# Performance work log

Hardware: AMD Instinct MI355X
Metric: run time of the kernel (lower is better)

## Reference

```python
import jax, jax.numpy as jnp
import numpy as np

D_CLAMP = 10.0
FAPE_EPS = 1e-4
Z = 10.0
TORSION_EPS = 1e-8


def backbone_fape(R_pred, t_pred, x_pred, R_true, t_true, x_true):
    # R_*: [B,N,3,3], t_*/x_*: [B,N,3]
    Rp_inv = jnp.swapaxes(R_pred, -1, -2)
    tp_inv = -jnp.einsum('birc,bic->bir', Rp_inv, t_pred)
    Rt_inv = jnp.swapaxes(R_true, -1, -2)
    tt_inv = -jnp.einsum('birc,bic->bir', Rt_inv, t_true)
    # [B,N,N,3] local-frame coordinates
    xf_pred = jnp.einsum('biop,bjp->bijo', Rp_inv, x_pred) + tp_inv[:, :, None, :]
    xf_true = jnp.einsum('biop,bjp->bijo', Rt_inv, x_true) + tt_inv[:, :, None, :]
    dist = jnp.sqrt(jnp.sum((xf_pred - xf_true) ** 2, axis=-1) + FAPE_EPS)
    dist = jnp.minimum(dist, D_CLAMP)
    return jnp.mean(dist, axis=(-1, -2)) / Z  # [B]


def torsion_angle_loss(pred, true, true_alt):
    # pred/true/true_alt: [B,N,7,2]
    norm = jnp.sqrt(jnp.sum(pred ** 2, axis=-1, keepdims=True) + TORSION_EPS)
    pred_n = pred / norm
    d_true = jnp.sqrt(jnp.sum((true - pred_n) ** 2, axis=-1, keepdims=True) + TORSION_EPS)
    d_alt = jnp.sqrt(jnp.sum((true_alt - pred_n) ** 2, axis=-1, keepdims=True) + TORSION_EPS)
    torsion = jnp.mean(jnp.minimum(d_true, d_alt), axis=(2, 3))  # [B,N]
    angle_norm = jnp.mean(jnp.abs(norm - 1.0), axis=(2, 3))      # [B,N]
    return torsion + 0.02 * angle_norm


def setup_inputs() -> dict:
    key = jax.random.key(0)
    ks = jax.random.split(key, 7)
    L, B, N = 8, 2, 2048
    return {
        'traj_rotations': jax.random.normal(ks[0], (L, B, N, 3, 3), jnp.float32),
        'traj_translations': jax.random.normal(ks[1], (L, B, N, 3), jnp.float32),
        'traj_torsions': jax.random.normal(ks[2], (L, B, N, 7, 2), jnp.float32),
        'true_rotations': jax.random.normal(ks[3], (B, N, 3, 3), jnp.float32),
        'true_translations': jax.random.normal(ks[4], (B, N, 3), jnp.float32),
        'true_torsion_angles': jax.random.normal(ks[5], (B, N, 7, 2), jnp.float32),
        'true_torsion_angles_alt': jax.random.normal(ks[6], (B, N, 7, 2), jnp.float32),
    }


def reference(traj_rotations, traj_translations, traj_torsions,
              true_rotations, true_translations,
              true_torsion_angles, true_torsion_angles_alt):
    num_layers = traj_rotations.shape[0]
    total = jnp.zeros(traj_rotations.shape[1], traj_rotations.dtype)
    for l in range(num_layers):  # small fixed layer count
        fape = backbone_fape(traj_rotations[l], traj_translations[l], traj_translations[l],
                             true_rotations, true_translations, true_translations)
        torsion = torsion_angle_loss(traj_torsions[l], true_torsion_angles,
                                     true_torsion_angles_alt).mean(axis=-1)
        total = total + fape + torsion
    return total / num_layers
```

## Files before the change

### kernel.cpp

```cpp
#include <hip/hip_runtime.h>
#include <math.h>

constexpr int L = 8;
constexpr int B = 2;
constexpr int N = 2048;
constexpr int LB = L * B;
constexpr int KF = 32;

constexpr float D_CLAMP2 = 100.0f;
constexpr float FAPE_EPS = 1e-4f;
constexpr float Z_CONST  = 10.0f;
constexpr float TEPS     = 1e-8f;

constexpr int THREADS = 256;
constexpr int IBLK    = 256;
constexpr int JCH     = 512;
constexpr int NIT     = N / IBLK;
constexpr int JSPLIT  = N / JCH;
constexpr int BLK_PER_LB  = NIT * JSPLIT;
constexpr int FAPE_BLOCKS = LB * BLK_PER_LB;
constexpr int TORS_PER_BLK = N / BLK_PER_LB;

typedef __attribute__((ext_vector_type(8))) short bf16x8;
typedef __attribute__((ext_vector_type(4))) float f32x4;

__device__ __forceinline__ float fast_sqrtf(float x) {
    return __builtin_amdgcn_sqrtf(x);
}
__device__ __forceinline__ unsigned cvt_pk(float lo, float hi) {
    unsigned r;
    asm("v_cvt_pk_bf16_f32 %0, %1, %2" : "=v"(r) : "v"(lo), "v"(hi));
    return r;
}
__device__ __forceinline__ float bf2f(unsigned short h) {
    return __uint_as_float((unsigned)h << 16);
}

__device__ __forceinline__ float wave_reduce_sum(float v) {
    #pragma unroll
    for (int off = 32; off > 0; off >>= 1)
        v += __shfl_down(v, off, 64);
    return v;
}

__device__ __forceinline__ float block_reduce_sum(float v) {
    __shared__ float s[4];
    v = wave_reduce_sum(v);
    int lane = threadIdx.x & 63;
    int w    = threadIdx.x >> 6;
    __syncthreads();
    if (lane == 0) s[w] = v;
    __syncthreads();
    return s[0] + s[1] + s[2] + s[3];
}

__device__ __forceinline__ void store_row(short* base, int r, const float* f) {
    #pragma unroll
    for (int c = 0; c < 4; ++c) {
        union { unsigned u[4]; bf16x8 v; } q;
        #pragma unroll
        for (int e = 0; e < 4; ++e)
            q.u[e] = cvt_pk(f[8 * c + 2 * e], f[8 * c + 2 * e + 1]);
        const int p = c ^ ((r >> 1) & 3);
        *(bf16x8*)(base + r * KF + p * 8) = q.v;
    }
}
__device__ __forceinline__ bf16x8 load_frag(const short* base, int r, int c) {
    const int p = c ^ ((r >> 1) & 3);
    return *(const bf16x8*)(base + r * KF + p * 8);
}

__global__ __launch_bounds__(THREADS)
void fape_all_kernel(const float* __restrict__ traj_rot,
                     const float* __restrict__ traj_trans,
                     const float* __restrict__ traj_tors,
                     const float* __restrict__ true_rot,
                     const float* __restrict__ true_trans,
                     const float* __restrict__ t_true,
                     const float* __restrict__ t_alt,
                     float* __restrict__ partials)
{
    __shared__ short phiL[JCH * KF];
    __shared__ short psiL[IBLK * KF];
    __shared__ float tors_s;

    const int bid = blockIdx.x;
    const int jh  = bid & (JSPLIT - 1);
    const int it  = (bid >> 2) & (NIT - 1);
    const int lb  = bid >> 5;
    const int b   = lb & (B - 1);
    const int tid = threadIdx.x;

    const float* tp = traj_trans + (size_t)lb * N * 3;
    const float* tt = true_trans + (size_t)b  * N * 3;

    #pragma unroll
    for (int half = 0; half < 2; ++half) {
        const int r = tid + half * THREADS;
        const int j = jh * JCH + r;
        float u[6] = { tp[3 * j], tp[3 * j + 1], tp[3 * j + 2],
                       tt[3 * j], tt[3 * j + 1], tt[3 * j + 2] };
        float phi[KF];
        #pragma unroll
        for (int c = 0; c < 6; ++c) phi[c] = u[c] * u[c];
        int idx = 6;
        #pragma unroll
        for (int c = 0; c < 6; ++c)
            #pragma unroll
            for (int d = c + 1; d < 6; ++d)
                phi[idx++] = u[c] * u[d];
        #pragma unroll
        for (int c = 0; c < 6; ++c) phi[21 + c] = u[c];
        phi[27] = 1.0f;
        phi[28] = 1.0f;
        phi[29] = phi[30] = phi[31] = 0.0f;
        store_row(phiL, r, phi);
    }

    {
        const int r = tid;
        const int i = it * IBLK + r;
        const float* Rp = traj_rot + ((size_t)lb * N + i) * 9;
        const float* Rt = true_rot + ((size_t)(b * N + i)) * 9;

        float W0[6], W1[6], W2[6];
        #pragma unroll
        for (int c = 0; c < 3; ++c) {
            W0[c] = Rp[3 * c];      W1[c] = Rp[3 * c + 1];      W2[c] = Rp[3 * c + 2];
            W0[c + 3] = -Rt[3 * c]; W1[c + 3] = -Rt[3 * c + 1]; W2[c + 3] = -Rt[3 * c + 2];
        }
        float u[6] = { tp[3 * i], tp[3 * i + 1], tp[3 * i + 2],
                       tt[3 * i], tt[3 * i + 1], tt[3 * i + 2] };

        float k0 = 0.f, k1 = 0.f, k2 = 0.f;
        #pragma unroll
        for (int c = 0; c < 6; ++c) {
            k0 = fmaf(W0[c], u[c], k0);
            k1 = fmaf(W1[c], u[c], k1);
            k2 = fmaf(W2[c], u[c], k2);
        }
        k0 = -k0; k1 = -k1; k2 = -k2;

        float psi[KF];
        #pragma unroll
        for (int c = 0; c < 6; ++c)
            psi[c] = fmaf(W0[c], W0[c], fmaf(W1[c], W1[c], W2[c] * W2[c]));
        int idx = 6;
        #pragma unroll
        for (int c = 0; c < 6; ++c)
            #pragma unroll
            for (int d = c + 1; d < 6; ++d)
                psi[idx++] = 2.0f * fmaf(W0[c], W0[d], fmaf(W1[c], W1[d], W2[c] * W2[d]));
        #pragma unroll
        for (int c = 0; c < 6; ++c)
            psi[21 + c] = 2.0f * fmaf(W0[c], k0, fmaf(W1[c], k1, W2[c] * k2));
        psi[27] = fmaf(k0, k0, fmaf(k1, k1, fmaf(k2, k2, FAPE_EPS)));
        psi[28] = psi[27] - bf2f((unsigned short)(cvt_pk(psi[27], psi[27]) & 0xffffu));
        psi[29] = psi[30] = psi[31] = 0.0f;
        store_row(psiL, r, psi);
    }

    if (tid < 64) {
        const int g  = lb * N + (bid & 31) * TORS_PER_BLK + tid;
        const int n  = g & (N - 1);
        const int bn = b * N + n;
        const float* p  = traj_tors + (size_t)g * 14;
        const float* tr = t_true + (size_t)bn * 14;
        const float* al = t_alt  + (size_t)bn * 14;

        float st = 0.0f, sa = 0.0f;
        #pragma unroll
        for (int k = 0; k < 7; ++k) {
            const float px = p[2 * k], py = p[2 * k + 1];
            const float nrm = fast_sqrtf(fmaf(px, px, fmaf(py, py, TEPS)));
            const float inv = __builtin_amdgcn_rcpf(nrm);
            const float pnx = px * inv, pny = py * inv;
            const float tx = tr[2 * k] - pnx, ty = tr[2 * k + 1] - pny;
            const float ax = al[2 * k] - pnx, ay = al[2 * k + 1] - pny;
            const float dt = fast_sqrtf(fmaf(tx, tx, fmaf(ty, ty, TEPS)));
            const float da = fast_sqrtf(fmaf(ax, ax, fmaf(ay, ay, TEPS)));
            st += fminf(dt, da);
            sa += fabsf(nrm - 1.0f);
        }
        float val = (st + 0.02f * sa) * (1.0f / 7.0f);
        val = wave_reduce_sum(val);
        if (tid == 0) tors_s = val;
    }

    __syncthreads();

    const int w    = tid >> 6;
    const int lane = tid & 63;
    const int wm   = w >> 1;
    const int wn   = w & 1;
    const int r15  = lane & 15;
    const int cch  = lane >> 4;

    bf16x8 a[8];
    #pragma unroll
    for (int s = 0; s < 8; ++s)
        a[s] = load_frag(psiL, wm * 128 + s * 16 + r15, cch);

    const f32x4 z = { 0.f, 0.f, 0.f, 0.f };
    float acc0 = 0.f, acc1 = 0.f, acc2 = 0.f, acc3 = 0.f;

    #pragma unroll
    for (int jp = 0; jp < 4; ++jp) {
        const int rb = wn * 256 + jp * 64 + r15;
        #pragma unroll
        for (int q = 0; q < 4; ++q) {
            const bf16x8 bq = load_frag(phiL, rb + q * 16, cch);
            f32x4 d[8];
            #pragma unroll
            for (int s = 0; s < 8; ++s)
                d[s] = __builtin_amdgcn_mfma_f32_16x16x32_bf16(a[s], bq, z, 0, 0, 0);
            #pragma unroll
            for (int s = 0; s < 8; ++s) {
                acc0 += fast_sqrtf(__builtin_amdgcn_fmed3f(d[s][0], 0.f, D_CLAMP2));
                acc1 += fast_sqrtf(__builtin_amdgcn_fmed3f(d[s][1], 0.f, D_CLAMP2));
                acc2 += fast_sqrtf(__builtin_amdgcn_fmed3f(d[s][2], 0.f, D_CLAMP2));
                acc3 += fast_sqrtf(__builtin_amdgcn_fmed3f(d[s][3], 0.f, D_CLAMP2));
            }
        }
    }

    const float tot = block_reduce_sum((acc0 + acc1) + (acc2 + acc3));
    if (tid == 0) {
        const float inv_pairs = 1.0f / ((float)N * (float)N * Z_CONST);
        partials[bid] = tot * inv_pairs + tors_s * (1.0f / (float)N);
    }
}

__global__ __launch_bounds__(THREADS)
void finalize_kernel(const float* __restrict__ partials,
                     float* __restrict__ out)
{
    float fs0 = 0.0f, fs1 = 0.0f;
    for (int t = threadIdx.x; t < FAPE_BLOCKS; t += THREADS) {
        const float v = partials[t];
        if ((t >> 5) & 1) fs1 += v; else fs0 += v;
    }
    const float F0 = block_reduce_sum(fs0);
    const float F1 = block_reduce_sum(fs1);
    if (threadIdx.x == 0) {
        out[0] = F0 / (float)L;
        out[1] = F1 / (float)L;
    }
}

extern "C" void kernel_launch(void* const* d_in, const int* in_sizes, int n_in,
                              void* d_out, int out_size, void* d_ws, size_t ws_size,
                              hipStream_t stream)
{
    const float* traj_rot   = (const float*)d_in[0];
    const float* traj_trans = (const float*)d_in[1];
    const float* traj_tors  = (const float*)d_in[2];
    const float* true_rot   = (const float*)d_in[3];
    const float* true_trans = (const float*)d_in[4];
    const float* true_ta    = (const float*)d_in[5];
    const float* true_taa   = (const float*)d_in[6];

    float* out      = (float*)d_out;
    float* partials = (float*)d_ws;

    fape_all_kernel<<<FAPE_BLOCKS, THREADS, 0, stream>>>(
        traj_rot, traj_trans, traj_tors, true_rot, true_trans,
        true_ta, true_taa, partials);
    finalize_kernel<<<1, THREADS, 0, stream>>>(partials, out);
}
```

Before: 20.61 us.

## Double block threads and reduce partials via fixed-point 64-bit atomics

Each block now runs 512 threads (8 waves) instead of 256, so each wave covers a smaller slice of the j range and per-thread phi row construction is halved. Per-block partial sums are scaled, quantized to 64-bit fixed point and atomically added per batch element, which keeps the result deterministic. The finalize kernel only converts those two accumulators back to float, and an async memset clears them first. The trade-offs are an extra memset launch, more waves competing for registers under the new launch bounds, and a small quantization error.

Result: slower. 24.67 us (+19.7%).

```diff
diff --git a/kernel.cpp b/kernel.cpp
--- a/kernel.cpp
+++ b/kernel.cpp
@@ -12,7 +12,7 @@
 constexpr float Z_CONST  = 10.0f;
 constexpr float TEPS     = 1e-8f;
 
-constexpr int THREADS = 256;
+constexpr int THREADS = 512;
 constexpr int IBLK    = 256;
 constexpr int JCH     = 512;
 constexpr int NIT     = N / IBLK;
@@ -21,6 +21,9 @@
 constexpr int FAPE_BLOCKS = LB * BLK_PER_LB;
 constexpr int TORS_PER_BLK = N / BLK_PER_LB;
 
+constexpr double ACC_SCALE  = 36028797018963968.0;
+constexpr double ACC_ISCALE = 1.0 / 36028797018963968.0;
+
 typedef __attribute__((ext_vector_type(8))) short bf16x8;
 typedef __attribute__((ext_vector_type(4))) float f32x4;
 
@@ -44,14 +47,17 @@
 }
 
 __device__ __forceinline__ float block_reduce_sum(float v) {
-    __shared__ float s[4];
+    __shared__ float s[8];
     v = wave_reduce_sum(v);
     int lane = threadIdx.x & 63;
     int w    = threadIdx.x >> 6;
     __syncthreads();
     if (lane == 0) s[w] = v;
     __syncthreads();
-    return s[0] + s[1] + s[2] + s[3];
+    float r = 0.f;
+    #pragma unroll
+    for (int k = 0; k < 8; ++k) r += s[k];
+    return r;
 }
 
 __device__ __forceinline__ void store_row(short* base, int r, const float* f) {
@@ -70,7 +76,7 @@
     return *(const bf16x8*)(base + r * KF + p * 8);
 }
 
-__global__ __launch_bounds__(THREADS)
+__global__ __launch_bounds__(THREADS, 4)
 void fape_all_kernel(const float* __restrict__ traj_rot,
                      const float* __restrict__ traj_trans,
                      const float* __restrict__ traj_tors,
@@ -78,7 +84,7 @@
                      const float* __restrict__ true_trans,
                      const float* __restrict__ t_true,
                      const float* __restrict__ t_alt,
-                     float* __restrict__ partials)
+                     unsigned long long* __restrict__ acc64)
 {
     __shared__ short phiL[JCH * KF];
     __shared__ short psiL[IBLK * KF];
@@ -94,9 +100,8 @@
     const float* tp = traj_trans + (size_t)lb * N * 3;
     const float* tt = true_trans + (size_t)b  * N * 3;
 
-    #pragma unroll
-    for (int half = 0; half < 2; ++half) {
-        const int r = tid + half * THREADS;
+    {
+        const int r = tid;
         const int j = jh * JCH + r;
         float u[6] = { tp[3 * j], tp[3 * j + 1], tp[3 * j + 2],
                        tt[3 * j], tt[3 * j + 1], tt[3 * j + 2] };
@@ -117,7 +122,7 @@
         store_row(phiL, r, phi);
     }
 
-    {
+    if (tid < IBLK) {
         const int r = tid;
         const int i = it * IBLK + r;
         const float* Rp = traj_rot + ((size_t)lb * N + i) * 9;
@@ -160,9 +165,10 @@
         store_row(psiL, r, psi);
     }
 
-    if (tid < 64) {
-        const int g  = lb * N + (bid & 31) * TORS_PER_BLK + tid;
-        const int n  = g & (N - 1);
+    if (tid >= 448) {
+        const int t  = tid - 448;
+        const int n  = (bid & 31) * TORS_PER_BLK + t;
+        const int g  = lb * N + n;
         const int bn = b * N + n;
         const float* p  = traj_tors + (size_t)g * 14;
         const float* tr = t_true + (size_t)bn * 14;
@@ -184,15 +190,15 @@
         }
         float val = (st + 0.02f * sa) * (1.0f / 7.0f);
         val = wave_reduce_sum(val);
-        if (tid == 0) tors_s = val;
+        if (tid == 448) tors_s = val;
     }
 
     __syncthreads();
 
     const int w    = tid >> 6;
     const int lane = tid & 63;
-    const int wm   = w >> 1;
-    const int wn   = w & 1;
+    const int wm   = w >> 2;
+    const int wn   = w & 3;
     const int r15  = lane & 15;
     const int cch  = lane >> 4;
 
@@ -205,47 +211,36 @@
     float acc0 = 0.f, acc1 = 0.f, acc2 = 0.f, acc3 = 0.f;
 
     #pragma unroll
-    for (int jp = 0; jp < 4; ++jp) {
-        const int rb = wn * 256 + jp * 64 + r15;
-        #pragma unroll
-        for (int q = 0; q < 4; ++q) {
-            const bf16x8 bq = load_frag(phiL, rb + q * 16, cch);
-            f32x4 d[8];
-            #pragma unroll
-            for (int s = 0; s < 8; ++s)
-                d[s] = __builtin_amdgcn_mfma_f32_16x16x32_bf16(a[s], bq, z, 0, 0, 0);
-            #pragma unroll
-            for (int s = 0; s < 8; ++s) {
-                acc0 += fast_sqrtf(__builtin_amdgcn_fmed3f(d[s][0], 0.f, D_CLAMP2));
-                acc1 += fast_sqrtf(__builtin_amdgcn_fmed3f(d[s][1], 0.f, D_CLAMP2));
-                acc2 += fast_sqrtf(__builtin_amdgcn_fmed3f(d[s][2], 0.f, D_CLAMP2));
-                acc3 += fast_sqrtf(__builtin_amdgcn_fmed3f(d[s][3], 0.f, D_CLAMP2));
-            }
+    for (int q = 0; q < 8; ++q) {
+        const bf16x8 bq = load_frag(phiL, wn * 128 + q * 16 + r15, cch);
+        f32x4 d[8];
+        #pragma unroll
+        for (int s = 0; s < 8; ++s)
+            d[s] = __builtin_amdgcn_mfma_f32_16x16x32_bf16(a[s], bq, z, 0, 0, 0);
+        #pragma unroll
+        for (int s = 0; s < 8; ++s) {
+            acc0 += fast_sqrtf(__builtin_amdgcn_fmed3f(d[s][0], 0.f, D_CLAMP2));
+            acc1 += fast_sqrtf(__builtin_amdgcn_fmed3f(d[s][1], 0.f, D_CLAMP2));
+            acc2 += fast_sqrtf(__builtin_amdgcn_fmed3f(d[s][2], 0.f, D_CLAMP2));
+            acc3 += fast_sqrtf(__builtin_amdgcn_fmed3f(d[s][3], 0.f, D_CLAMP2));
         }
     }
 
     const float tot = block_reduce_sum((acc0 + acc1) + (acc2 + acc3));
     if (tid == 0) {
-        const float inv_pairs = 1.0f / ((float)N * (float)N * Z_CONST);
-        partials[bid] = tot * inv_pairs + tors_s * (1.0f / (float)N);
-    }
-}
-
-__global__ __launch_bounds__(THREADS)
-void finalize_kernel(const float* __restrict__ partials,
-                     float* __restrict__ out)
+        const float partial = tot * (1.0f / ((float)N * (float)N * Z_CONST * (float)L))
+                            + tors_s * (1.0f / ((float)N * (float)L));
+        const unsigned long long q =
+            (unsigned long long)(long long)((double)partial * ACC_SCALE + 0.5);
+        atomicAdd(&acc64[b], q);
+    }
+}
+
+__global__ void finalize_kernel(const unsigned long long* __restrict__ acc64,
+                                float* __restrict__ out)
 {
-    float fs0 = 0.0f, fs1 = 0.0f;
-    for (int t = threadIdx.x; t < FAPE_BLOCKS; t += THREADS) {
-        const float v = partials[t];
-        if ((t >> 5) & 1) fs1 += v; else fs0 += v;
-    }
-    const float F0 = block_reduce_sum(fs0);
-    const float F1 = block_reduce_sum(fs1);
-    if (threadIdx.x == 0) {
-        out[0] = F0 / (float)L;
-        out[1] = F1 / (float)L;
-    }
+    if (threadIdx.x < B)
+        out[threadIdx.x] = (float)((double)acc64[threadIdx.x] * ACC_ISCALE);
 }
 
 extern "C" void kernel_launch(void* const* d_in, const int* in_sizes, int n_in,
@@ -260,11 +255,13 @@
     const float* true_ta    = (const float*)d_in[5];
     const float* true_taa   = (const float*)d_in[6];
 
-    float* out      = (float*)d_out;
-    float* partials = (float*)d_ws;
+    float* out = (float*)d_out;
+    unsigned long long* acc64 = (unsigned long long*)d_ws;
+
+    hipMemsetAsync(acc64, 0, B * sizeof(unsigned long long), stream);
 
     fape_all_kernel<<<FAPE_BLOCKS, THREADS, 0, stream>>>(
         traj_rot, traj_trans, traj_tors, true_rot, true_trans,
-        true_ta, true_taa, partials);
-    finalize_kernel<<<1, THREADS, 0, stream>>>(partials, out);
-}
+        true_ta, true_taa, acc64);
+    finalize_kernel<<<1, 64, 0, stream>>>(acc64, out);
+}
```
